# Kernel optimization log

Hardware: AMD Instinct MI355X
Metric: run time of the kernel (lower is better)

## Reference

```python
import jax, jax.numpy as jnp
import numpy as np

B, S, H, V_SZ = 256, 49, 2048, 10000

def setup_inputs() -> dict:
    key = jax.random.key(0)
    ks = jax.random.split(key, 24)
    sc = 0.02
    inp = {
        'V': jax.random.normal(ks[0], (B, S, H), jnp.float32),
        'v_g': jax.random.normal(ks[1], (B, H), jnp.float32),
        'state': jax.random.normal(ks[2], (2, 1, B, H), jnp.float32),
        'captions': jax.random.randint(ks[3], (B, 16), 0, V_SZ, jnp.int32),
        'time': 1,
        # params (torch Linear convention: W is (out,in), y = x@W.T+b)
        'fc_W': jax.random.normal(ks[4], (H, H), jnp.float32) * sc,
        'fc_b': jnp.zeros((H,), jnp.float32),
        'att_W': jax.random.normal(ks[5], (H, H), jnp.float32) * sc,
        'att_b': jnp.zeros((H,), jnp.float32),
        'emb': jax.random.normal(ks[6], (V_SZ + 1, H), jnp.float32) * sc,
        'ctx_W': jax.random.normal(ks[7], (H, H), jnp.float32) * sc,
        'ctx_b': jnp.zeros((H,), jnp.float32),
        'a2c_W': jax.random.normal(ks[8], (2 * H, H), jnp.float32) * sc,
        'a2c_b': jnp.zeros((2 * H,), jnp.float32),
        'i2h_W': jax.random.normal(ks[9], (5 * H, H), jnp.float32) * sc,
        'i2h_b': jnp.zeros((5 * H,), jnp.float32),
        'h2h_W': jax.random.normal(ks[10], (5 * H, H), jnp.float32) * sc,
        'h2h_b': jnp.zeros((5 * H,), jnp.float32),
        'h2att_W': jax.random.normal(ks[11], (H, H), jnp.float32) * sc,
        'h2att_b': jnp.zeros((H,), jnp.float32),
        'alpha_W': jax.random.normal(ks[12], (1, H), jnp.float32) * sc,
        'alpha_b': jnp.zeros((1,), jnp.float32),
    }
    return inp


def reference(V, v_g, state, fc_W, fc_b, att_W, att_b, emb, ctx_W, ctx_b,
              a2c_W, a2c_b, i2h_W, i2h_b, h2h_W, h2h_b,
              h2att_W, h2att_b, alpha_W, alpha_b, captions, time):
    # fc_embed(v_g): computed by the original module (unused downstream)
    fc_feats = jax.nn.relu(v_g @ fc_W.T + fc_b)
    # att_embed + ctx2att over the 49 spatial locations
    att_feats = jax.nn.relu(jnp.einsum('bsf,hf->bsh', V, att_W) + att_b)   # (B,49,H)
    p_att = jnp.einsum('bsh,ah->bsa', att_feats, ctx_W) + ctx_b            # (B,49,H)
    # word embedding
    it = captions[:, time]
    xt = jax.nn.relu(emb[it])                                              # (B,H)
    if time == 0:
        state = jnp.zeros_like(state)
    h_prev, c_prev = state[0, -1], state[1, -1]                            # (B,H) each
    # Bahdanau attention
    att_h = h_prev @ h2att_W.T + h2att_b                                   # (B,H)
    dot = jnp.tanh(p_att + att_h[:, None, :])                              # (B,49,H)
    scores = jnp.einsum('bsh,h->bs', dot, alpha_W[0]) + alpha_b[0]         # (B,49)
    weight = jax.nn.softmax(scores, axis=1)
    att_res = jnp.einsum('bs,bsh->bh', weight, att_feats)                  # (B,H)
    # LSTM-with-maxout cell
    sums = xt @ i2h_W.T + i2h_b + h_prev @ h2h_W.T + h2h_b                 # (B,5H)
    Hd = h_prev.shape[-1]
    gates = jax.nn.sigmoid(sums[:, :3 * Hd])
    in_gate, forget_gate, out_gate = gates[:, :Hd], gates[:, Hd:2 * Hd], gates[:, 2 * Hd:]
    in_tr = sums[:, 3 * Hd:] + (att_res @ a2c_W.T + a2c_b)                 # (B,2H)
    in_tr = jnp.maximum(in_tr[:, :Hd], in_tr[:, Hd:])                      # maxout
    next_c = forget_gate * c_prev + in_gate * in_tr
    next_h = out_gate * jnp.tanh(next_c)
    output = next_h[:, None, :]                                            # (B,1,H)
    return output, next_h[None], next_c[None]
```

## Files before the change

### kernel.cpp

```cpp
#include <hip/hip_runtime.h>


typedef __bf16 bf16x8 __attribute__((ext_vector_type(8)));
typedef float  f32x4  __attribute__((ext_vector_type(4)));

static constexpr int Bn = 256;
static constexpr int Sn = 49;
static constexpr int Hn = 2048;
static constexpr int Mrows = Bn * Sn;
static constexpr int LDP = 72;

__device__ __forceinline__ unsigned short f2bf(float f) {
    unsigned u = __builtin_bit_cast(unsigned, f);
    u += 0x7FFFu + ((u >> 16) & 1u);
    return (unsigned short)(u >> 16);
}
__device__ __forceinline__ float bf2f(unsigned short h) {
    return __builtin_bit_cast(float, ((unsigned)h) << 16);
}

__global__ void k_convert(const float* __restrict__ src,
                          unsigned short* __restrict__ dst, int n8) {
    int i = blockIdx.x * blockDim.x + threadIdx.x;
    if (i >= n8) return;
    const float4* p = (const float4*)src + (size_t)i * 2;
    float4 a = p[0], b = p[1];
    union { unsigned short us[8]; int4 v; } o;
    o.us[0] = f2bf(a.x); o.us[1] = f2bf(a.y); o.us[2] = f2bf(a.z); o.us[3] = f2bf(a.w);
    o.us[4] = f2bf(b.x); o.us[5] = f2bf(b.y); o.us[6] = f2bf(b.z); o.us[7] = f2bf(b.w);
    ((int4*)dst)[i] = o.v;
}

__global__ void k_gather(const float* __restrict__ emb,
                         const float* __restrict__ state,
                         const int* __restrict__ captions,
                         const int* __restrict__ timep,
                         unsigned short* __restrict__ xt_b,
                         unsigned short* __restrict__ h_b) {
    int b = blockIdx.x;
    int tm = timep[0];
    int it = captions[b * 16 + tm];
    const float* erow = emb + (size_t)it * Hn;
    for (int h = threadIdx.x; h < Hn; h += blockDim.x) {
        float x = erow[h];
        xt_b[(size_t)b * Hn + h] = f2bf(x > 0.f ? x : 0.f);
        float hv = (tm == 0) ? 0.f : state[(size_t)b * Hn + h];
        h_b[(size_t)b * Hn + h] = f2bf(hv);
    }
}

template<int EPI>
__global__ __launch_bounds__(512, 1)
void k_gemm8(const unsigned short* __restrict__ A,
             const unsigned short* __restrict__ B,
             const float* __restrict__ bias, void* __restrict__ out,
             const float* __restrict__ atth, const float* __restrict__ alphaW,
             int M, int N, int K) {
    __shared__ __align__(16) unsigned short lds[2][2][2][128 * 64];

    const int tid  = threadIdx.x;
    const int lane = tid & 63;
    const int wave = tid >> 6;
    const int wm = wave >> 2;
    const int wn = wave & 3;
    const int wh = wn >> 1;

    const int nm = M >> 8;
    const int wg = (blockIdx.x & 7) * nm + (blockIdx.x >> 3);
    const int m_tile = wg % nm, n_tile = wg / nm;
    const size_t am0 = (size_t)m_tile * 256;
    const size_t bn0 = (size_t)n_tile * 256;

    const int srow = lane >> 3;
    const int scol = (((lane & 7) ^ srow)) * 8;

#define STG(SLOT, G, RBASE, KT)                                              \
    {                                                                        \
        _Pragma("unroll")                                                    \
        for (int j_ = 0; j_ < 2; ++j_) {                                     \
            const int rr_ = (wave * 2 + j_) * 8 + srow;                      \
            const unsigned short* src_ =                                     \
                (G) + ((RBASE) + rr_) * (size_t)K + (KT) * 64 + scol;        \
            __builtin_amdgcn_global_load_lds(                                \
                (const __attribute__((address_space(1))) void*)src_,         \
                (__attribute__((address_space(3))) void*)((SLOT) + (wave * 2 + j_) * 512), \
                16, 0, 0);                                                   \
        }                                                                    \
    }

    unsigned short* SA0_0 = &lds[0][0][0][0];
    unsigned short* SA0_1 = &lds[0][0][1][0];
    unsigned short* SB0_0 = &lds[0][1][0][0];
    unsigned short* SB0_1 = &lds[0][1][1][0];
    unsigned short* SA1_0 = &lds[1][0][0][0];
    unsigned short* SA1_1 = &lds[1][0][1][0];
    unsigned short* SB1_0 = &lds[1][1][0][0];
    unsigned short* SB1_1 = &lds[1][1][1][0];

    const unsigned short* As0r = &lds[0][0][wm][0];
    const unsigned short* As1r = &lds[1][0][wm][0];
    const unsigned short* Bs0r = &lds[0][1][wh][0];
    const unsigned short* Bs1r = &lds[1][1][wh][0];

    const int rfrag = lane & 15;
    const int wnl = (wn & 1) * 64;
    const int ck0 = (((lane >> 4) * 8)) ^ ((lane & 7) * 8);
    const int ck1 = (32 + ((lane >> 4) * 8)) ^ ((lane & 7) * 8);

    f32x4 acc[8][4];
#pragma unroll
    for (int m = 0; m < 8; ++m)
#pragma unroll
        for (int n = 0; n < 4; ++n)
#pragma unroll
            for (int r = 0; r < 4; ++r) acc[m][n][r] = 0.f;

    bf16x8 bfr[4][2], pf0[2][2], pf1[2][2];

#define RDA(ASR, TP, PF)                                                     \
    _Pragma("unroll")                                                        \
    for (int mm = 0; mm < 2; ++mm) {                                         \
        PF[mm][0] = *(const bf16x8*)&(ASR)[((2 * (TP) + mm) * 16 + rfrag) * 64 + ck0]; \
        PF[mm][1] = *(const bf16x8*)&(ASR)[((2 * (TP) + mm) * 16 + rfrag) * 64 + ck1]; \
    }
#define RDB(BSR)                                                             \
    _Pragma("unroll")                                                        \
    for (int n = 0; n < 4; ++n) {                                            \
        bfr[n][0] = *(const bf16x8*)&(BSR)[(wnl + n * 16 + rfrag) * 64 + ck0]; \
        bfr[n][1] = *(const bf16x8*)&(BSR)[(wnl + n * 16 + rfrag) * 64 + ck1]; \
    }
#define MM(PF, TP)                                                           \
    __builtin_amdgcn_s_setprio(1);                                           \
    _Pragma("unroll")                                                        \
    for (int mm = 0; mm < 2; ++mm)                                           \
        _Pragma("unroll")                                                    \
        for (int n = 0; n < 4; ++n)                                          \
            _Pragma("unroll")                                                \
            for (int s = 0; s < 2; ++s)                                      \
                acc[2 * (TP) + mm][n] = __builtin_amdgcn_mfma_f32_16x16x32_bf16( \
                    PF[mm][s], bfr[n][s], acc[2 * (TP) + mm][n], 0, 0, 0);   \
    __builtin_amdgcn_s_setprio(0);

#define FENCE  __builtin_amdgcn_sched_barrier(0)
#define LGKM0  asm volatile("s_waitcnt lgkmcnt(0)" ::: "memory")
#define VM4    asm volatile("s_waitcnt vmcnt(4)" ::: "memory")
#define BAR    __builtin_amdgcn_s_barrier()

    STG(SB0_0, B, bn0 + 0,   0);
    STG(SB0_1, B, bn0 + 128, 0);
    STG(SA0_0, A, am0 + 0,   0);
    STG(SA0_1, A, am0 + 128, 0);
    asm volatile("s_waitcnt vmcnt(0)" ::: "memory");
    BAR;
    RDB(Bs0r);
    RDA(As0r, 0, pf0);
    STG(SB1_0, B, bn0 + 0,   1);
    STG(SB1_1, B, bn0 + 128, 1);
    STG(SA1_0, A, am0 + 0,   1);
    STG(SA1_1, A, am0 + 128, 1);
    LGKM0;
    BAR;

    const int KT_MAX = K / 64 - 1;
    for (int it = 0; it < K / 128; ++it) {
        const int ktP2 = (2 * it + 2 < KT_MAX) ? 2 * it + 2 : KT_MAX;
        const int ktQ3 = (2 * it + 3 < KT_MAX) ? 2 * it + 3 : KT_MAX;
        RDA(As0r, 1, pf1); FENCE;
        MM(pf0, 0);
        LGKM0; FENCE;
        STG(SB0_0, B, bn0 + 0, ktP2);
        BAR;
        RDA(As0r, 2, pf0); FENCE;
        MM(pf1, 1);
        LGKM0; FENCE;
        STG(SB0_1, B, bn0 + 128, ktP2);
        BAR;
        RDA(As0r, 3, pf1); FENCE;
        MM(pf0, 2);
        LGKM0; FENCE;
        VM4;
        BAR;
        RDA(As1r, 0, pf0); FENCE;
        MM(pf1, 3);
        RDB(Bs1r); FENCE;
        LGKM0; FENCE;
        STG(SA0_0, A, am0 + 0, ktP2);
        BAR;
        RDA(As1r, 1, pf1); FENCE;
        MM(pf0, 0);
        LGKM0; FENCE;
        STG(SA0_1, A, am0 + 128, ktP2);
        STG(SB1_0, B, bn0 + 0, ktQ3);
        BAR;
        RDA(As1r, 2, pf0); FENCE;
        MM(pf1, 1);
        LGKM0; FENCE;
        STG(SB1_1, B, bn0 + 128, ktQ3);
        BAR;
        RDA(As1r, 3, pf1); FENCE;
        MM(pf0, 2);
        LGKM0; FENCE;
        VM4;
        BAR;
        RDA(As0r, 0, pf0); FENCE;
        MM(pf1, 3);
        RDB(Bs0r); FENCE;
        LGKM0; FENCE;
        STG(SA1_0, A, am0 + 0, ktQ3);
        STG(SA1_1, A, am0 + 128, ktQ3);
        BAR;
    }
#undef STG
#undef RDA
#undef RDB
#undef MM

    asm volatile("s_waitcnt vmcnt(0)" ::: "memory");

    const int rq = (lane >> 4) << 2;
#pragma unroll
    for (int m = 0; m < 8; ++m) {
#pragma unroll
        for (int r = 0; r < 4; ++r) {
            const size_t gm = am0 + (size_t)wm * 128 + m * 16 + rq + r;
            if constexpr (EPI == 3) {
                float partial = 0.f;
                const int b = (int)(gm / Sn);
#pragma unroll
                for (int n = 0; n < 4; ++n) {
                    const int gn = (int)bn0 + wn * 64 + n * 16 + rfrag;
                    float v = acc[m][n][r] + bias[gn] + atth[(size_t)b * N + gn];
                    partial += tanhf(v) * alphaW[gn];
                }
#pragma unroll
                for (int off = 1; off < 16; off <<= 1)
                    partial += __shfl_xor(partial, off);
                if (rfrag == 0) atomicAdd(&((float*)out)[gm], partial);
            } else {
#pragma unroll
                for (int n = 0; n < 4; ++n) {
                    const int gn = (int)bn0 + wn * 64 + n * 16 + rfrag;
                    float v = acc[m][n][r] + bias[gn];
                    ((unsigned short*)out)[gm * N + gn] = f2bf(v > 0.f ? v : 0.f);
                }
            }
        }
    }
}

template<bool DUAL>
__global__ __launch_bounds__(256)
void k_gemm_s(const unsigned short* __restrict__ A, const float* __restrict__ B,
              const unsigned short* __restrict__ A2, const float* __restrict__ B2,
              const float* __restrict__ bias, const float* __restrict__ bias2,
              float* __restrict__ out, int M, int N, int K) {
    __shared__ __align__(16) unsigned short As[128 * LDP];
    __shared__ __align__(16) unsigned short Bs[128 * LDP];

    const int tid = threadIdx.x;
    const int m0 = blockIdx.y * 128;
    const int n0 = blockIdx.x * 128;
    const int lane = tid & 63;
    const int wave = tid >> 6;
    const int wm = (wave >> 1) * 64;
    const int wn = (wave & 1) * 64;

    f32x4 acc[4][4];
#pragma unroll
    for (int i = 0; i < 4; ++i)
#pragma unroll
        for (int j = 0; j < 4; ++j)
#pragma unroll
            for (int r = 0; r < 4; ++r) acc[i][j][r] = 0.f;

    const int npass = DUAL ? 2 : 1;
    for (int pass = 0; pass < npass; ++pass) {
        const unsigned short* Ap = pass ? A2 : A;
        const float* Bp = pass ? B2 : B;
        for (int kt = 0; kt < K; kt += 64) {
            __syncthreads();
            {
                const int r = tid >> 3, c = (tid & 7) << 3;
                const unsigned short* src = Ap + (size_t)(m0 + r) * K + kt + c;
#pragma unroll
                for (int i = 0; i < 4; ++i) {
                    int4 v = *(const int4*)(src + (size_t)i * 32 * K);
                    *(int4*)&As[(r + i * 32) * LDP + c] = v;
                }
            }
            {
                const int r = tid >> 4, c = (tid & 15) << 2;
                const float* src = Bp + (size_t)(n0 + r) * K + kt + c;
#pragma unroll
                for (int i = 0; i < 8; ++i) {
                    float4 v = *(const float4*)(src + (size_t)i * 16 * K);
                    union { unsigned short us[4]; uint2 u2; } t;
                    t.us[0] = f2bf(v.x); t.us[1] = f2bf(v.y);
                    t.us[2] = f2bf(v.z); t.us[3] = f2bf(v.w);
                    *(uint2*)&Bs[(r + i * 16) * LDP + c] = t.u2;
                }
            }
            __syncthreads();
#pragma unroll
            for (int ks = 0; ks < 64; ks += 32) {
                const int col = ks + ((lane >> 4) << 3);
                const int ra = wm + (lane & 15);
                const int rb = wn + (lane & 15);
                bf16x8 af[4], bfr[4];
#pragma unroll
                for (int i = 0; i < 4; ++i)
                    af[i] = *(const bf16x8*)&As[(ra + i * 16) * LDP + col];
#pragma unroll
                for (int j = 0; j < 4; ++j)
                    bfr[j] = *(const bf16x8*)&Bs[(rb + j * 16) * LDP + col];
#pragma unroll
                for (int i = 0; i < 4; ++i)
#pragma unroll
                    for (int j = 0; j < 4; ++j)
                        acc[i][j] = __builtin_amdgcn_mfma_f32_16x16x32_bf16(
                            af[i], bfr[j], acc[i][j], 0, 0, 0);
            }
        }
    }

#pragma unroll
    for (int i = 0; i < 4; ++i) {
#pragma unroll
        for (int r = 0; r < 4; ++r) {
            const int gm = m0 + wm + i * 16 + ((lane >> 4) << 2) + r;
#pragma unroll
            for (int j = 0; j < 4; ++j) {
                const int gn = n0 + wn + j * 16 + (lane & 15);
                float v = acc[i][j][r] + bias[gn];
                if (DUAL) v += bias2[gn];
                out[(size_t)gm * N + gn] = v;
            }
        }
    }
}

__global__ void k_softmax(const float* __restrict__ scores, float* __restrict__ weight) {
    int b = blockIdx.x;
    int s = threadIdx.x;
    float v = (s < Sn) ? scores[b * Sn + s] : -1e30f;
    float m = v;
#pragma unroll
    for (int off = 1; off < 64; off <<= 1) m = fmaxf(m, __shfl_xor(m, off));
    float e = (s < Sn) ? __expf(v - m) : 0.f;
    float sum = e;
#pragma unroll
    for (int off = 1; off < 64; off <<= 1) sum += __shfl_xor(sum, off);
    if (s < Sn) weight[b * Sn + s] = e / sum;
}

__global__ void k_attres(const float* __restrict__ weight,
                         const unsigned short* __restrict__ attf,
                         unsigned short* __restrict__ attres) {
    int b = blockIdx.y;
    int h = blockIdx.x * blockDim.x + threadIdx.x;
    const unsigned short* p = attf + (size_t)b * Sn * Hn + h;
    float acc = 0.f;
#pragma unroll 7
    for (int s = 0; s < Sn; ++s)
        acc += weight[b * Sn + s] * bf2f(p[(size_t)s * Hn]);
    attres[(size_t)b * Hn + h] = f2bf(acc);
}

__global__ void k_final(const float* __restrict__ sums, const float* __restrict__ a2c,
                        const float* __restrict__ state, const int* __restrict__ timep,
                        float* __restrict__ out) {
    int idx = blockIdx.x * blockDim.x + threadIdx.x;
    int b = idx >> 11, h = idx & (Hn - 1);
    const float* srow = sums + (size_t)b * 5 * Hn;
    float ig = 1.f / (1.f + __expf(-srow[h]));
    float fg = 1.f / (1.f + __expf(-srow[Hn + h]));
    float og = 1.f / (1.f + __expf(-srow[2 * Hn + h]));
    float t1 = srow[3 * Hn + h] + a2c[(size_t)b * 2 * Hn + h];
    float t2 = srow[4 * Hn + h] + a2c[(size_t)b * 2 * Hn + Hn + h];
    float intr = fmaxf(t1, t2);
    float cprev = (timep[0] == 0) ? 0.f : state[(size_t)Bn * Hn + idx];
    float c = fg * cprev + ig * intr;
    float hh = og * tanhf(c);
    const int BH = Bn * Hn;
    out[idx] = hh;
    out[BH + idx] = hh;
    out[2 * BH + idx] = c;
}

extern "C" void kernel_launch(void* const* d_in, const int* in_sizes, int n_in,
                              void* d_out, int out_size, void* d_ws, size_t ws_size,
                              hipStream_t stream) {
    const float* V        = (const float*)d_in[0];
    const float* state    = (const float*)d_in[2];
    const int*   captions = (const int*)d_in[3];
    const int*   timep    = (const int*)d_in[4];
    const float* att_W    = (const float*)d_in[7];
    const float* att_b    = (const float*)d_in[8];
    const float* emb      = (const float*)d_in[9];
    const float* ctx_W    = (const float*)d_in[10];
    const float* ctx_b    = (const float*)d_in[11];
    const float* a2c_W    = (const float*)d_in[12];
    const float* a2c_b    = (const float*)d_in[13];
    const float* i2h_W    = (const float*)d_in[14];
    const float* i2h_b    = (const float*)d_in[15];
    const float* h2h_W    = (const float*)d_in[16];
    const float* h2h_b    = (const float*)d_in[17];
    const float* h2att_W  = (const float*)d_in[18];
    const float* h2att_b  = (const float*)d_in[19];
    const float* alpha_W  = (const float*)d_in[20];

    unsigned short* Vb      = (unsigned short*)d_ws;
    unsigned short* attWb   = Vb + (size_t)Mrows * Hn;
    unsigned short* ctxWb   = attWb + (size_t)Hn * Hn;
    unsigned short* attfb   = ctxWb + (size_t)Hn * Hn;
    unsigned short* xtb     = attfb + (size_t)Mrows * Hn;
    unsigned short* hb      = xtb + Bn * Hn;
    unsigned short* attresb = hb + Bn * Hn;
    float* atth    = (float*)(attresb + Bn * Hn);
    float* scores  = atth + Bn * Hn;
    float* weight  = scores + Mrows;
    float* sums    = weight + Mrows;
    float* a2c_out = sums + (size_t)Bn * 5 * Hn;

    hipMemsetAsync(scores, 0, Mrows * sizeof(float), stream);

    k_convert<<<(Mrows * Hn / 8) / 256, 256, 0, stream>>>(V, Vb, Mrows * Hn / 8);
    k_convert<<<(Hn * Hn / 8) / 256, 256, 0, stream>>>(att_W, attWb, Hn * Hn / 8);
    k_convert<<<(Hn * Hn / 8) / 256, 256, 0, stream>>>(ctx_W, ctxWb, Hn * Hn / 8);
    k_gather<<<Bn, 256, 0, stream>>>(emb, state, captions, timep, xtb, hb);

    const int nwg = (Mrows / 256) * (Hn / 256);

    k_gemm8<0><<<nwg, 512, 0, stream>>>(
        Vb, attWb, att_b, attfb, nullptr, nullptr, Mrows, Hn, Hn);
    k_gemm_s<false><<<dim3(Hn / 128, Bn / 128), 256, 0, stream>>>(
        hb, h2att_W, nullptr, nullptr, h2att_b, nullptr, atth, Bn, Hn, Hn);
    k_gemm8<3><<<nwg, 512, 0, stream>>>(
        attfb, ctxWb, ctx_b, scores, atth, alpha_W, Mrows, Hn, Hn);
    k_softmax<<<Bn, 64, 0, stream>>>(scores, weight);
    k_attres<<<dim3(Hn / 256, Bn), 256, 0, stream>>>(weight, attfb, attresb);
    k_gemm_s<true><<<dim3(5 * Hn / 128, Bn / 128), 256, 0, stream>>>(
        xtb, i2h_W, hb, h2h_W, i2h_b, h2h_b, sums, Bn, 5 * Hn, Hn);
    k_gemm_s<false><<<dim3(2 * Hn / 128, Bn / 128), 256, 0, stream>>>(
        attresb, a2c_W, nullptr, nullptr, a2c_b, nullptr, a2c_out, Bn, 2 * Hn, Hn);

    k_final<<<Bn * Hn / 256, 256, 0, stream>>>(sums, a2c_out, state, timep, (float*)d_out);
}
```

Before: 558.5 us.

## Merge conversion launches, co-schedule small GEMMs, fuse softmax into attention reduce

The three fp32-to-bf16 conversion launches become one kernel that branches on index range. The h2att GEMM and the dual i2h/h2h GEMM now run in a single launch (96x2 blocks), which removes a launch and fills more CUs early. The softmax kernel is folded into the attention-weighted sum kernel, where each thread recomputes max, sum and exp from the 49 scores. This saves two launches and the weight buffer, at the cost of redundant exp work per thread and an unbalanced mixed GEMM grid.

```diff
diff --git a/kernel.cpp b/kernel.cpp
--- a/kernel.cpp
+++ b/kernel.cpp
@@ -19,10 +19,15 @@
     return __builtin_bit_cast(float, ((unsigned)h) << 16);
 }
 
-__global__ void k_convert(const float* __restrict__ src,
-                          unsigned short* __restrict__ dst, int n8) {
+__global__ void k_convert3(const float* __restrict__ s0, unsigned short* __restrict__ d0, int n0,
+                           const float* __restrict__ s1, unsigned short* __restrict__ d1, int n1,
+                           const float* __restrict__ s2, unsigned short* __restrict__ d2, int n2) {
     int i = blockIdx.x * blockDim.x + threadIdx.x;
-    if (i >= n8) return;
+    const float* src; unsigned short* dst;
+    if (i < n0)            { src = s0; dst = d0; }
+    else if (i < n0 + n1)  { src = s1; dst = d1; i -= n0; }
+    else if (i < n0 + n1 + n2) { src = s2; dst = d2; i -= n0 + n1; }
+    else return;
     const float4* p = (const float4*)src + (size_t)i * 2;
     float4 a = p[0], b = p[1];
     union { unsigned short us[8]; int4 v; } o;
@@ -248,11 +253,107 @@
     }
 }
 
-template<bool DUAL>
+__global__ __launch_bounds__(256)
+void k_gemm_pre(const unsigned short* __restrict__ xtb,
+                const unsigned short* __restrict__ hb,
+                const float* __restrict__ i2h_W, const float* __restrict__ h2h_W,
+                const float* __restrict__ h2att_W,
+                const float* __restrict__ i2h_b, const float* __restrict__ h2h_b,
+                const float* __restrict__ h2att_b,
+                float* __restrict__ sums, float* __restrict__ atth) {
+    __shared__ __align__(16) unsigned short As[128 * LDP];
+    __shared__ __align__(16) unsigned short Bs[128 * LDP];
+
+    const int K = Hn;
+    const bool isPre = blockIdx.x < 80;
+    const int n0 = (isPre ? blockIdx.x : (blockIdx.x - 80)) * 128;
+    const int Nld = isPre ? 5 * Hn : Hn;
+    float* outp = isPre ? sums : atth;
+
+    const int tid = threadIdx.x;
+    const int m0 = blockIdx.y * 128;
+    const int lane = tid & 63;
+    const int wave = tid >> 6;
+    const int wm = (wave >> 1) * 64;
+    const int wn = (wave & 1) * 64;
+
+    f32x4 acc[4][4];
+#pragma unroll
+    for (int i = 0; i < 4; ++i)
+#pragma unroll
+        for (int j = 0; j < 4; ++j)
+#pragma unroll
+            for (int r = 0; r < 4; ++r) acc[i][j][r] = 0.f;
+
+    const int npass = isPre ? 2 : 1;
+    for (int pass = 0; pass < npass; ++pass) {
+        const unsigned short* Ap = pass ? hb : (isPre ? xtb : hb);
+        const float* Bp = pass ? h2h_W : (isPre ? i2h_W : h2att_W);
+        for (int kt = 0; kt < K; kt += 64) {
+            __syncthreads();
+            {
+                const int r = tid >> 3, c = (tid & 7) << 3;
+                const unsigned short* src = Ap + (size_t)(m0 + r) * K + kt + c;
+#pragma unroll
+                for (int i = 0; i < 4; ++i) {
+                    int4 v = *(const int4*)(src + (size_t)i * 32 * K);
+                    *(int4*)&As[(r + i * 32) * LDP + c] = v;
+                }
+            }
+            {
+                const int r = tid >> 4, c = (tid & 15) << 2;
+                const float* src = Bp + (size_t)(n0 + r) * K + kt + c;
+#pragma unroll
+                for (int i = 0; i < 8; ++i) {
+                    float4 v = *(const float4*)(src + (size_t)i * 16 * K);
+                    union { unsigned short us[4]; uint2 u2; } t;
+                    t.us[0] = f2bf(v.x); t.us[1] = f2bf(v.y);
+                    t.us[2] = f2bf(v.z); t.us[3] = f2bf(v.w);
+                    *(uint2*)&Bs[(r + i * 16) * LDP + c] = t.u2;
+                }
+            }
+            __syncthreads();
+#pragma unroll
+            for (int ks = 0; ks < 64; ks += 32) {
+                const int col = ks + ((lane >> 4) << 3);
+                const int ra = wm + (lane & 15);
+                const int rb = wn + (lane & 15);
+                bf16x8 af[4], bfr[4];
+#pragma unroll
+                for (int i = 0; i < 4; ++i)
+                    af[i] = *(const bf16x8*)&As[(ra + i * 16) * LDP + col];
+#pragma unroll
+                for (int j = 0; j < 4; ++j)
+                    bfr[j] = *(const bf16x8*)&Bs[(rb + j * 16) * LDP + col];
+#pragma unroll
+                for (int i = 0; i < 4; ++i)
+#pragma unroll
+                    for (int j = 0; j < 4; ++j)
+                        acc[i][j] = __builtin_amdgcn_mfma_f32_16x16x32_bf16(
+                            af[i], bfr[j], acc[i][j], 0, 0, 0);
+            }
+        }
+    }
+
+#pragma unroll
+    for (int i = 0; i < 4; ++i) {
+#pragma unroll
+        for (int r = 0; r < 4; ++r) {
+            const int gm = m0 + wm + i * 16 + ((lane >> 4) << 2) + r;
+#pragma unroll
+            for (int j = 0; j < 4; ++j) {
+                const int gn = n0 + wn + j * 16 + (lane & 15);
+                float v = acc[i][j][r] +
+                          (isPre ? (i2h_b[gn] + h2h_b[gn]) : h2att_b[gn]);
+                outp[(size_t)gm * Nld + gn] = v;
+            }
+        }
+    }
+}
+
 __global__ __launch_bounds__(256)
 void k_gemm_s(const unsigned short* __restrict__ A, const float* __restrict__ B,
-              const unsigned short* __restrict__ A2, const float* __restrict__ B2,
-              const float* __restrict__ bias, const float* __restrict__ bias2,
+              const float* __restrict__ bias,
               float* __restrict__ out, int M, int N, int K) {
     __shared__ __align__(16) unsigned short As[128 * LDP];
     __shared__ __align__(16) unsigned short Bs[128 * LDP];
@@ -273,53 +374,48 @@
 #pragma unroll
             for (int r = 0; r < 4; ++r) acc[i][j][r] = 0.f;
 
-    const int npass = DUAL ? 2 : 1;
-    for (int pass = 0; pass < npass; ++pass) {
-        const unsigned short* Ap = pass ? A2 : A;
-        const float* Bp = pass ? B2 : B;
-        for (int kt = 0; kt < K; kt += 64) {
-            __syncthreads();
-            {
-                const int r = tid >> 3, c = (tid & 7) << 3;
-                const unsigned short* src = Ap + (size_t)(m0 + r) * K + kt + c;
-#pragma unroll
-                for (int i = 0; i < 4; ++i) {
-                    int4 v = *(const int4*)(src + (size_t)i * 32 * K);
-                    *(int4*)&As[(r + i * 32) * LDP + c] = v;
-                }
-            }
-            {
-                const int r = tid >> 4, c = (tid & 15) << 2;
-                const float* src = Bp + (size_t)(n0 + r) * K + kt + c;
-#pragma unroll
-                for (int i = 0; i < 8; ++i) {
-                    float4 v = *(const float4*)(src + (size_t)i * 16 * K);
-                    union { unsigned short us[4]; uint2 u2; } t;
-                    t.us[0] = f2bf(v.x); t.us[1] = f2bf(v.y);
-                    t.us[2] = f2bf(v.z); t.us[3] = f2bf(v.w);
-                    *(uint2*)&Bs[(r + i * 16) * LDP + c] = t.u2;
-                }
-            }
-            __syncthreads();
-#pragma unroll
-            for (int ks = 0; ks < 64; ks += 32) {
-                const int col = ks + ((lane >> 4) << 3);
-                const int ra = wm + (lane & 15);
-                const int rb = wn + (lane & 15);
-                bf16x8 af[4], bfr[4];
-#pragma unroll
-                for (int i = 0; i < 4; ++i)
-                    af[i] = *(const bf16x8*)&As[(ra + i * 16) * LDP + col];
+    for (int kt = 0; kt < K; kt += 64) {
+        __syncthreads();
+        {
+            const int r = tid >> 3, c = (tid & 7) << 3;
+            const unsigned short* src = A + (size_t)(m0 + r) * K + kt + c;
+#pragma unroll
+            for (int i = 0; i < 4; ++i) {
+                int4 v = *(const int4*)(src + (size_t)i * 32 * K);
+                *(int4*)&As[(r + i * 32) * LDP + c] = v;
+            }
+        }
+        {
+            const int r = tid >> 4, c = (tid & 15) << 2;
+            const float* src = B + (size_t)(n0 + r) * K + kt + c;
+#pragma unroll
+            for (int i = 0; i < 8; ++i) {
+                float4 v = *(const float4*)(src + (size_t)i * 16 * K);
+                union { unsigned short us[4]; uint2 u2; } t;
+                t.us[0] = f2bf(v.x); t.us[1] = f2bf(v.y);
+                t.us[2] = f2bf(v.z); t.us[3] = f2bf(v.w);
+                *(uint2*)&Bs[(r + i * 16) * LDP + c] = t.u2;
+            }
+        }
+        __syncthreads();
+#pragma unroll
+        for (int ks = 0; ks < 64; ks += 32) {
+            const int col = ks + ((lane >> 4) << 3);
+            const int ra = wm + (lane & 15);
+            const int rb = wn + (lane & 15);
+            bf16x8 af[4], bfr[4];
+#pragma unroll
+            for (int i = 0; i < 4; ++i)
+                af[i] = *(const bf16x8*)&As[(ra + i * 16) * LDP + col];
+#pragma unroll
+            for (int j = 0; j < 4; ++j)
+                bfr[j] = *(const bf16x8*)&Bs[(rb + j * 16) * LDP + col];
+#pragma unroll
+            for (int i = 0; i < 4; ++i)
 #pragma unroll
                 for (int j = 0; j < 4; ++j)
-                    bfr[j] = *(const bf16x8*)&Bs[(rb + j * 16) * LDP + col];
-#pragma unroll
-                for (int i = 0; i < 4; ++i)
-#pragma unroll
-                    for (int j = 0; j < 4; ++j)
-                        acc[i][j] = __builtin_amdgcn_mfma_f32_16x16x32_bf16(
-                            af[i], bfr[j], acc[i][j], 0, 0, 0);
-            }
+                    acc[i][j] = __builtin_amdgcn_mfma_f32_16x16x32_bf16(
+                        af[i], bfr[j], acc[i][j], 0, 0, 0);
         }
     }
 
@@ -331,39 +427,31 @@
 #pragma unroll
             for (int j = 0; j < 4; ++j) {
                 const int gn = n0 + wn + j * 16 + (lane & 15);
-                float v = acc[i][j][r] + bias[gn];
-                if (DUAL) v += bias2[gn];
-                out[(size_t)gm * N + gn] = v;
-            }
-        }
-    }
-}
-
-__global__ void k_softmax(const float* __restrict__ scores, float* __restrict__ weight) {
-    int b = blockIdx.x;
-    int s = threadIdx.x;
-    float v = (s < Sn) ? scores[b * Sn + s] : -1e30f;
-    float m = v;
-#pragma unroll
-    for (int off = 1; off < 64; off <<= 1) m = fmaxf(m, __shfl_xor(m, off));
-    float e = (s < Sn) ? __expf(v - m) : 0.f;
-    float sum = e;
-#pragma unroll
-    for (int off = 1; off < 64; off <<= 1) sum += __shfl_xor(sum, off);
-    if (s < Sn) weight[b * Sn + s] = e / sum;
-}
-
-__global__ void k_attres(const float* __restrict__ weight,
-                         const unsigned short* __restrict__ attf,
-                         unsigned short* __restrict__ attres) {
+                out[(size_t)gm * N + gn] = acc[i][j][r] + bias[gn];
+            }
+        }
+    }
+}
+
+__global__ void k_attres_sm(const float* __restrict__ scores,
+                            const unsigned short* __restrict__ attf,
+                            unsigned short* __restrict__ attres) {
     int b = blockIdx.y;
     int h = blockIdx.x * blockDim.x + threadIdx.x;
+    const float* sc = scores + b * Sn;
+    float m = -1e30f;
+#pragma unroll 7
+    for (int s = 0; s < Sn; ++s) m = fmaxf(m, sc[s]);
+    float sum = 0.f;
+#pragma unroll 7
+    for (int s = 0; s < Sn; ++s) sum += __expf(sc[s] - m);
+    const float inv = 1.f / sum;
     const unsigned short* p = attf + (size_t)b * Sn * Hn + h;
     float acc = 0.f;
 #pragma unroll 7
     for (int s = 0; s < Sn; ++s)
-        acc += weight[b * Sn + s] * bf2f(p[(size_t)s * Hn]);
-    attres[(size_t)b * Hn + h] = f2bf(acc);
+        acc += __expf(sc[s] - m) * bf2f(p[(size_t)s * Hn]);
+    attres[(size_t)b * Hn + h] = f2bf(acc * inv);
 }
 
 __global__ void k_final(const float* __restrict__ sums, const float* __restrict__ a2c,
@@ -424,25 +512,22 @@
 
     hipMemsetAsync(scores, 0, Mrows * sizeof(float), stream);
 
-    k_convert<<<(Mrows * Hn / 8) / 256, 256, 0, stream>>>(V, Vb, Mrows * Hn / 8);
-    k_convert<<<(Hn * Hn / 8) / 256, 256, 0, stream>>>(att_W, attWb, Hn * Hn / 8);
-    k_convert<<<(Hn * Hn / 8) / 256, 256, 0, stream>>>(ctx_W, ctxWb, Hn * Hn / 8);
+    const int nc0 = Mrows * Hn / 8, nc1 = Hn * Hn / 8, nc2 = Hn * Hn / 8;
+    k_convert3<<<(nc0 + nc1 + nc2 + 255) / 256, 256, 0, stream>>>(
+        V, Vb, nc0, att_W, attWb, nc1, ctx_W, ctxWb, nc2);
     k_gather<<<Bn, 256, 0, stream>>>(emb, state, captions, timep, xtb, hb);
 
     const int nwg = (Mrows / 256) * (Hn / 256);
 
     k_gemm8<0><<<nwg, 512, 0, stream>>>(
         Vb, attWb, att_b, attfb, nullptr, nullptr, Mrows, Hn, Hn);
-    k_gemm_s<false><<<dim3(Hn / 128, Bn / 128), 256, 0, stream>>>(
-        hb, h2att_W, nullptr, nullptr, h2att_b, nullptr, atth, Bn, Hn, Hn);
+    k_gemm_pre<<<dim3(96, 2), 256, 0, stream>>>(
+        xtb, hb, i2h_W, h2h_W, h2att_W, i2h_b, h2h_b, h2att_b, sums, atth);
     k_gemm8<3><<<nwg, 512, 0, stream>>>(
         attfb, ctxWb, ctx_b, scores, atth, alpha_W, Mrows, Hn, Hn);
-    k_softmax<<<Bn, 64, 0, stream>>>(scores, weight);
-    k_attres<<<dim3(Hn / 256, Bn), 256, 0, stream>>>(weight, attfb, attresb);
-    k_gemm_s<true><<<dim3(5 * Hn / 128, Bn / 128), 256, 0, stream>>>(
-        xtb, i2h_W, hb, h2h_W, i2h_b, h2h_b, sums, Bn, 5 * Hn, Hn);
-    k_gemm_s<false><<<dim3(2 * Hn / 128, Bn / 128), 256, 0, stream>>>(
-        attresb, a2c_W, nullptr, nullptr, a2c_b, nullptr, a2c_out, Bn, 2 * Hn, Hn);
+    k_attres_sm<<<dim3(Hn / 256, Bn), 256, 0, stream>>>(scores, attfb, attresb);
+    k_gemm_s<<<dim3(2 * Hn / 128, Bn / 128), 256, 0, stream>>>(
+        attresb, a2c_W, a2c_b, a2c_out, Bn, 2 * Hn, Hn);
 
     k_final<<<Bn * Hn / 256, 256, 0, stream>>>(sums, a2c_out, state, timep, (float*)d_out);
 }
```

Result: faster. 525.9 us (-5.9%).
